# Kernel tuning notes

Measured on AMD Instinct MI355X. Metric: run time of the kernel, lower is better.

Reference implementation:

```python
import jax, jax.numpy as jnp
import numpy as np

B, S, D_MODEL = 2, 2048, 1024
HEADS = 16
DK = D_MODEL // HEADS  # 64
Q_RANK, RANK = 6, 2
ROPE_BASE = 10000.0


def _xavier(key, shape):
    # torch nn.init.xavier_uniform_ on weight (out,in); stored here as (in,out)
    fan_in, fan_out = shape
    a = (6.0 / (fan_in + fan_out)) ** 0.5
    return jax.random.uniform(key, shape, jnp.float32, -a, a)


def setup_inputs() -> dict:
    key = jax.random.key(0)
    ks = jax.random.split(key, 10)
    inp = {
        "q": jax.random.normal(ks[0], (B, S, D_MODEL), jnp.float32),
        "k": jax.random.normal(ks[1], (B, S, D_MODEL), jnp.float32),
        "v": jax.random.normal(ks[2], (B, S, D_MODEL), jnp.float32),
        # causal mask; mask==0 -> -inf in scores
        "mask": jnp.tril(jnp.ones((S, S), dtype=bool))[None, None],
        "W_Aq": _xavier(ks[3], (D_MODEL, Q_RANK * HEADS)),
        "W_Ak": _xavier(ks[4], (D_MODEL, RANK * HEADS)),
        "W_Av": _xavier(ks[5], (D_MODEL, RANK * HEADS)),
        "W_Bq": _xavier(ks[6], (D_MODEL, Q_RANK * DK)),
        "W_Bk": _xavier(ks[7], (D_MODEL, RANK * DK)),
        "W_Bv": _xavier(ks[8], (D_MODEL, RANK * DK)),
        "Wo": _xavier(ks[9], (D_MODEL, D_MODEL)),
    }
    return inp


def _rotary_cos_sin(seq_len, dim):
    inv_freq = 1.0 / (ROPE_BASE ** (jnp.arange(0, dim, 2, dtype=jnp.float32) / dim))
    freqs = jnp.outer(jnp.arange(seq_len, dtype=jnp.float32), inv_freq)  # [S, dim/2]
    return jnp.cos(freqs)[None, :, None, :], jnp.sin(freqs)[None, :, None, :]


def _apply_rotary(x, cos, sin):
    # x: [B, S, R, dk]; rotate-half style RoPE
    d = x.shape[-1] // 2
    x1, x2 = x[..., :d], x[..., d:]
    return jnp.concatenate([x1 * cos + x2 * sin, -x1 * sin + x2 * cos], axis=-1)


def reference(q, k, v, mask, W_Aq, W_Ak, W_Av, W_Bq, W_Bk, W_Bv, Wo):
    Bn, Sn, D = q.shape
    # low-rank factor projections
    A_q = (q @ W_Aq).reshape(Bn, Sn, HEADS, Q_RANK)
    A_k = (k @ W_Ak).reshape(Bn, Sn, HEADS, RANK)
    A_v = (v @ W_Av).reshape(Bn, Sn, HEADS, RANK)
    B_q = (q @ W_Bq).reshape(Bn, Sn, Q_RANK, DK)
    B_k = (k @ W_Bk).reshape(Bn, Sn, RANK, DK)
    B_v = (v @ W_Bv).reshape(Bn, Sn, RANK, DK)
    cos, sin = _rotary_cos_sin(Sn, DK)
    B_q = _apply_rotary(B_q, cos, sin)
    B_k = _apply_rotary(B_k, cos, sin)
    # reconstruct per-head q/k/v: [B,H,S,dk]
    qh = jnp.einsum("bshr,bsrd->bhsd", A_q, B_q) / Q_RANK
    kh = jnp.einsum("bshr,bsrd->bhsd", A_k, B_k) / RANK
    vh = jnp.einsum("bshr,bsrd->bhsd", A_v, B_v) / RANK
    # NOTE: original divides by d_k (not sqrt(d_k)) -- faithful to source
    score = jnp.einsum("bhqd,bhkd->bhqk", qh, kh) / DK
    score = jnp.where(mask, score, -jnp.inf)
    # dropout is identity (eval / dropout=0.0)
    att = jax.nn.softmax(score, axis=-1)
    out = jnp.einsum("bhqk,bhkd->bqhd", att, vh).reshape(Bn, Sn, D)
    return out @ Wo
```

## Files before the change

kernel.cpp:

```cpp
#include <hip/hip_runtime.h>
#include <hip/hip_bf16.h>


typedef __attribute__((ext_vector_type(8))) short short8;
typedef __attribute__((ext_vector_type(4))) float floatx4;

#define MFMA16(a, b, c) __builtin_amdgcn_mfma_f32_16x16x32_bf16(a, b, c, 0, 0, 0)

__device__ __forceinline__ float b2f(short s) {
    unsigned int u = ((unsigned int)(unsigned short)s) << 16;
    float f; __builtin_memcpy(&f, &u, 4); return f;
}
__device__ __forceinline__ unsigned short bfbits(float x) {
    __hip_bfloat16 h = __float2bfloat16(x);
    unsigned short u; __builtin_memcpy(&u, &h, 2); return u;
}

__device__ __forceinline__ float wsrc(int n, int k,
                                      const float* __restrict__ Aq, const float* __restrict__ Bq,
                                      const float* __restrict__ Ak, const float* __restrict__ Bk,
                                      const float* __restrict__ Av, const float* __restrict__ Bv,
                                      const float* __restrict__ Wo) {
    if (n < 96) return Aq[(size_t)k * 96 + n];
    if (n < 480) return Bq[(size_t)k * 384 + (n - 96)];
    if (n < 512) return 0.f;
    if (n < 544) return Ak[(size_t)k * 32 + (n - 512)];
    if (n < 672) return Bk[(size_t)k * 128 + (n - 544)];
    if (n < 768) return 0.f;
    if (n < 800) return Av[(size_t)k * 32 + (n - 768)];
    if (n < 928) return Bv[(size_t)k * 128 + (n - 800)];
    if (n < 1024) return 0.f;
    return Wo[(size_t)k * 1024 + (n - 1024)];
}

__global__ __launch_bounds__(256) void pack_wT_kernel(const float* __restrict__ Aq,
                                                      const float* __restrict__ Bq,
                                                      const float* __restrict__ Ak,
                                                      const float* __restrict__ Bk,
                                                      const float* __restrict__ Av,
                                                      const float* __restrict__ Bv,
                                                      const float* __restrict__ Wo,
                                                      __hip_bfloat16* __restrict__ outBase) {
    __shared__ float tile[64][65];
    int k0 = blockIdx.x * 64, n0 = blockIdx.y * 64;
    int tid = threadIdx.x;
#pragma unroll
    for (int p = 0; p < 16; ++p) {
        int idx = p * 256 + tid;
        int kl = idx >> 6, nl = idx & 63;
        tile[kl][nl] = wsrc(n0 + nl, k0 + kl, Aq, Bq, Ak, Bk, Av, Bv, Wo);
    }
    __syncthreads();
#pragma unroll
    for (int p = 0; p < 16; ++p) {
        int idx = p * 256 + tid;
        int nl = idx >> 6, kl = idx & 63;
        outBase[(size_t)(n0 + nl) * 1024 + k0 + kl] = __float2bfloat16(tile[kl][nl]);
    }
}

__global__ __launch_bounds__(256) void gemm3_kernel(const float* __restrict__ q,
                                                    const float* __restrict__ k,
                                                    const float* __restrict__ v,
                                                    const __hip_bfloat16* __restrict__ WT,
                                                    __hip_bfloat16* __restrict__ Pq,
                                                    __hip_bfloat16* __restrict__ Pk,
                                                    __hip_bfloat16* __restrict__ Pv) {
    __shared__ __align__(16) __hip_bfloat16 As[128][72];
    __shared__ __align__(16) __hip_bfloat16 Bs[128][72];
    int lin = blockIdx.x;
    int t = (lin >> 3) & 7;
    int m0 = ((lin & 7) + ((lin >> 6) << 3)) * 128;
    const float* A; __hip_bfloat16* C; int N, n0, wrow;
    if (t < 4)      { A = q; C = Pq; N = 512; n0 = t * 128;        wrow = t * 128; }
    else if (t < 6) { A = k; C = Pk; N = 256; n0 = (t - 4) * 128;  wrow = 512 + (t - 4) * 128; }
    else            { A = v; C = Pv; N = 256; n0 = (t - 6) * 128;  wrow = 768 + (t - 6) * 128; }
    int tid = threadIdx.x;
    int wave = tid >> 6, lane = tid & 63, quad = lane >> 4, l15 = lane & 15;
    int wm = wave >> 1, wn = wave & 1;
    floatx4 acc[4][4];
#pragma unroll
    for (int mt = 0; mt < 4; ++mt)
#pragma unroll
        for (int nt = 0; nt < 4; ++nt) acc[mt][nt] = (floatx4){0.f, 0.f, 0.f, 0.f};

    for (int k0 = 0; k0 < 1024; k0 += 64) {
#pragma unroll
        for (int pp = 0; pp < 8; ++pp) {
            int idx = pp * 256 + tid;
            int row = idx >> 4, c4 = (idx & 15) * 4;
            float4 av = *(const float4*)(A + (size_t)(m0 + row) * 1024 + k0 + c4);
            ushort4 bv;
            bv.x = bfbits(av.x); bv.y = bfbits(av.y); bv.z = bfbits(av.z); bv.w = bfbits(av.w);
            *(ushort4*)&As[row][c4] = bv;
        }
#pragma unroll
        for (int pp = 0; pp < 4; ++pp) {
            int idx = pp * 256 + tid;
            int row = idx >> 3, c8 = (idx & 7) * 8;
            *(uint4*)&Bs[row][c8] = *(const uint4*)(WT + (size_t)(wrow + row) * 1024 + k0 + c8);
        }
        __syncthreads();
#pragma unroll
        for (int ks = 0; ks < 64; ks += 32) {
            short8 af[4], bf[4];
#pragma unroll
            for (int t2 = 0; t2 < 4; ++t2) {
                af[t2] = *(const short8*)&As[wm * 64 + t2 * 16 + l15][ks + quad * 8];
                bf[t2] = *(const short8*)&Bs[wn * 64 + t2 * 16 + l15][ks + quad * 8];
            }
#pragma unroll
            for (int mt = 0; mt < 4; ++mt)
#pragma unroll
                for (int nt = 0; nt < 4; ++nt)
                    acc[mt][nt] = MFMA16(af[mt], bf[nt], acc[mt][nt]);
        }
        __syncthreads();
    }
#pragma unroll
    for (int mt = 0; mt < 4; ++mt)
#pragma unroll
        for (int nt = 0; nt < 4; ++nt)
#pragma unroll
            for (int r = 0; r < 4; ++r) {
                int row = m0 + wm * 64 + mt * 16 + quad * 4 + r;
                int col = n0 + wn * 64 + nt * 16 + l15;
                C[(size_t)row * N + col] = __float2bfloat16(acc[mt][nt][r]);
            }
}

__global__ __launch_bounds__(256) void gemm_out_kernel(const __hip_bfloat16* __restrict__ A,
                                                       const __hip_bfloat16* __restrict__ BT,
                                                       float* __restrict__ C) {
    __shared__ __align__(16) __hip_bfloat16 As[128][72];
    __shared__ __align__(16) __hip_bfloat16 Bs[128][72];
    int lin = blockIdx.x;
    int n0 = ((lin >> 3) & 7) * 128;
    int m0 = ((lin & 7) + ((lin >> 6) << 3)) * 128;
    int tid = threadIdx.x;
    int wave = tid >> 6, lane = tid & 63, quad = lane >> 4, l15 = lane & 15;
    int wm = wave >> 1, wn = wave & 1;
    floatx4 acc[4][4];
#pragma unroll
    for (int mt = 0; mt < 4; ++mt)
#pragma unroll
        for (int nt = 0; nt < 4; ++nt) acc[mt][nt] = (floatx4){0.f, 0.f, 0.f, 0.f};

    for (int k0 = 0; k0 < 1024; k0 += 64) {
#pragma unroll
        for (int pp = 0; pp < 4; ++pp) {
            int idx = pp * 256 + tid;
            int row = idx >> 3, c8 = (idx & 7) * 8;
            *(uint4*)&As[row][c8] = *(const uint4*)(A + (size_t)(m0 + row) * 1024 + k0 + c8);
            *(uint4*)&Bs[row][c8] = *(const uint4*)(BT + (size_t)(n0 + row) * 1024 + k0 + c8);
        }
        __syncthreads();
#pragma unroll
        for (int ks = 0; ks < 64; ks += 32) {
            short8 af[4], bf[4];
#pragma unroll
            for (int t2 = 0; t2 < 4; ++t2) {
                af[t2] = *(const short8*)&As[wm * 64 + t2 * 16 + l15][ks + quad * 8];
                bf[t2] = *(const short8*)&Bs[wn * 64 + t2 * 16 + l15][ks + quad * 8];
            }
#pragma unroll
            for (int mt = 0; mt < 4; ++mt)
#pragma unroll
                for (int nt = 0; nt < 4; ++nt)
                    acc[mt][nt] = MFMA16(af[mt], bf[nt], acc[mt][nt]);
        }
        __syncthreads();
    }
#pragma unroll
    for (int mt = 0; mt < 4; ++mt)
#pragma unroll
        for (int nt = 0; nt < 4; ++nt)
#pragma unroll
            for (int r = 0; r < 4; ++r) {
                int row = m0 + wm * 64 + mt * 16 + quad * 4 + r;
                int col = n0 + wn * 64 + nt * 16 + l15;
                C[(size_t)row * 1024 + col] = acc[mt][nt][r];
            }
}

__global__ __launch_bounds__(256) void combine_vt_kernel(const __hip_bfloat16* __restrict__ Pq,
                                                         const __hip_bfloat16* __restrict__ Pk,
                                                         const __hip_bfloat16* __restrict__ Pv,
                                                         __hip_bfloat16* __restrict__ qh,
                                                         __hip_bfloat16* __restrict__ kh,
                                                         __hip_bfloat16* __restrict__ vT) {
    __shared__ __align__(16) __hip_bfloat16 LAq[16][96];
    __shared__ __align__(16) __hip_bfloat16 LAk[16][32];
    __shared__ __align__(16) __hip_bfloat16 LAv[16][32];
    __shared__ __align__(16) __hip_bfloat16 LBq[16][6][72];
    __shared__ __align__(16) __hip_bfloat16 LBk[16][2][72];
    __shared__ __align__(16) __hip_bfloat16 LBv[16][2][72];
    int tid = threadIdx.x;
    int token0 = blockIdx.x * 16;
    int b = token0 >> 11, s0 = token0 & 2047, bh0 = b * 16;

    for (int i = tid; i < 16 * 512; i += 256) {
        int s = i >> 9, c = i & 511;
        __hip_bfloat16 val = Pq[(size_t)(token0 + s) * 512 + c];
        if (c < 96) LAq[s][c] = val;
        else if (c < 480) LBq[s][(c - 96) >> 6][(c - 96) & 63] = val;
    }
    for (int i = tid; i < 16 * 256; i += 256) {
        int s = i >> 8, c = i & 255;
        __hip_bfloat16 vk = Pk[(size_t)(token0 + s) * 256 + c];
        __hip_bfloat16 vv = Pv[(size_t)(token0 + s) * 256 + c];
        if (c < 32) { LAk[s][c] = vk; LAv[s][c] = vv; }
        else if (c < 160) {
            LBk[s][(c - 32) >> 6][(c - 32) & 63] = vk;
            LBv[s][(c - 32) >> 6][(c - 32) & 63] = vv;
        }
    }
    __syncthreads();
    for (int i = tid; i < 4096; i += 256) {
        int s = i >> 8, rr = (i >> 5) & 7, d = i & 31;
        float inv = __expf(-(float)d * 0.28782313662425576f);
        float rev = (float)(s0 + s) * inv * 0.15915494309189535f;
        rev -= floorf(rev);
        float sn = __builtin_amdgcn_sinf(rev);
        float cs = __builtin_amdgcn_cosf(rev);
        if (rr < 6) {
            float x1 = b2f(*(short*)&LBq[s][rr][d]), x2 = b2f(*(short*)&LBq[s][rr][d + 32]);
            LBq[s][rr][d] = __float2bfloat16(x1 * cs + x2 * sn);
            LBq[s][rr][d + 32] = __float2bfloat16(-x1 * sn + x2 * cs);
        } else {
            int r2 = rr - 6;
            float x1 = b2f(*(short*)&LBk[s][r2][d]), x2 = b2f(*(short*)&LBk[s][r2][d + 32]);
            LBk[s][r2][d] = __float2bfloat16(x1 * cs + x2 * sn);
            LBk[s][r2][d + 32] = __float2bfloat16(-x1 * sn + x2 * cs);
        }
    }
    __syncthreads();
    const float QSCALE = 1.4426950408889634f / 768.0f;
    {
        int s = tid >> 4, h = tid & 15;
        float aq[6], ak0, ak1;
#pragma unroll
        for (int r = 0; r < 6; ++r) aq[r] = b2f(*(short*)&LAq[s][h * 6 + r]);
        ak0 = b2f(*(short*)&LAk[s][h * 2]);
        ak1 = b2f(*(short*)&LAk[s][h * 2 + 1]);
        size_t obase = ((size_t)(bh0 + h) * 2048 + s0 + s) * 64;
#pragma unroll
        for (int dc = 0; dc < 64; dc += 8) {
            float accq[8] = {0, 0, 0, 0, 0, 0, 0, 0};
#pragma unroll
            for (int r = 0; r < 6; ++r) {
                short8 bq = *(const short8*)&LBq[s][r][dc];
#pragma unroll
                for (int e = 0; e < 8; ++e) accq[e] += aq[r] * b2f(bq[e]);
            }
            short8 bk0 = *(const short8*)&LBk[s][0][dc];
            short8 bk1 = *(const short8*)&LBk[s][1][dc];
            ushort outq[8], outk[8];
#pragma unroll
            for (int e = 0; e < 8; ++e) {
                outq[e] = bfbits(accq[e] * QSCALE);
                outk[e] = bfbits(ak0 * b2f(bk0[e]) + ak1 * b2f(bk1[e]));
            }
            *(uint4*)((__hip_bfloat16*)qh + obase + dc) = *(uint4*)outq;
            *(uint4*)((__hip_bfloat16*)kh + obase + dc) = *(uint4*)outk;
        }
    }
    {
        int s = tid & 15, dg = tid >> 4;
#pragma unroll
        for (int h = 0; h < 16; ++h) {
            float a0 = b2f(*(short*)&LAv[s][h * 2]) * 0.5f;
            float a1 = b2f(*(short*)&LAv[s][h * 2 + 1]) * 0.5f;
#pragma unroll
            for (int dd = 0; dd < 4; ++dd) {
                int d = dg * 4 + dd;
                float val = a0 * b2f(*(short*)&LBv[s][0][d]) + a1 * b2f(*(short*)&LBv[s][1][d]);
                vT[((size_t)(bh0 + h) * 64 + d) * 2048 + s0 + s] = __float2bfloat16(val);
            }
        }
    }
}

__global__ __launch_bounds__(256) void flash_kernel(const __hip_bfloat16* __restrict__ qh,
                                                    const __hip_bfloat16* __restrict__ kh,
                                                    const __hip_bfloat16* __restrict__ vT,
                                                    __hip_bfloat16* __restrict__ att) {
    int lin = blockIdx.x + (blockIdx.y << 5);
    int bh = ((lin & 7) << 2) | ((lin >> 3) & 3);
    int qi = 31 - (lin >> 5);
    int tid = threadIdx.x;
    int wave = tid >> 6, lane = tid & 63, quad = lane >> 4, l15 = lane & 15;
    int q0 = qi * 64;
    __shared__ __align__(16) __hip_bfloat16 Ks[64][72];
    __shared__ __align__(16) __hip_bfloat16 Vts[64][72];

    const __hip_bfloat16* qrow = qh + ((size_t)bh * 2048 + q0 + wave * 16 + l15) * 64 + quad * 8;
    short8 aq0 = *(const short8*)(qrow);
    short8 aq1 = *(const short8*)(qrow + 32);

    floatx4 o[4];
#pragma unroll
    for (int nt = 0; nt < 4; ++nt) o[nt] = (floatx4){0.f, 0.f, 0.f, 0.f};
    float rs = 0.f;
    int qloc = wave * 16 + l15;

    for (int j = 0; j <= qi; ++j) {
        int k0 = j * 64;
#pragma unroll
        for (int pp = 0; pp < 2; ++pp) {
            int idx = pp * 256 + tid;
            int row = idx >> 3, c8 = (idx & 7) * 8;
            *(uint4*)&Ks[row][c8] = *(const uint4*)(kh + ((size_t)bh * 2048 + k0 + row) * 64 + c8);
            *(uint4*)&Vts[row][c8] = *(const uint4*)(vT + ((size_t)bh * 64 + row) * 2048 + k0 + c8);
        }
        __syncthreads();

        floatx4 s[4];
#pragma unroll
        for (int nt = 0; nt < 4; ++nt) s[nt] = (floatx4){0.f, 0.f, 0.f, 0.f};
#pragma unroll
        for (int nt = 0; nt < 4; ++nt) {
            short8 bk0 = *(const short8*)&Ks[nt * 16 + l15][quad * 8];
            short8 bk1 = *(const short8*)&Ks[nt * 16 + l15][32 + quad * 8];
            s[nt] = MFMA16(bk0, aq0, s[nt]);
            s[nt] = MFMA16(bk1, aq1, s[nt]);
        }
        if (j == qi) {
#pragma unroll
            for (int nt = 0; nt < 4; ++nt) {
                int kbase = nt * 16 + quad * 4;
#pragma unroll
                for (int r = 0; r < 4; ++r)
                    if (kbase + r > qloc) s[nt][r] = -__builtin_inff();
            }
        }
        float pv[4][4];
#pragma unroll
        for (int nt = 0; nt < 4; ++nt)
#pragma unroll
            for (int r = 0; r < 4; ++r) {
                pv[nt][r] = exp2f(s[nt][r]);
                rs += pv[nt][r];
            }
        union { ushort u[8]; short8 v; } p0, p1;
#pragma unroll
        for (int r = 0; r < 4; ++r) {
            p0.u[r]     = bfbits(pv[0][r]);
            p0.u[4 + r] = bfbits(pv[1][r]);
            p1.u[r]     = bfbits(pv[2][r]);
            p1.u[4 + r] = bfbits(pv[3][r]);
        }
#pragma unroll
        for (int nt = 0; nt < 4; ++nt) {
            int vr = nt * 16 + l15;
            union { ushort4 h[2]; short8 v; } x0, x1;
            x0.h[0] = *(const ushort4*)&Vts[vr][quad * 4];
            x0.h[1] = *(const ushort4*)&Vts[vr][16 + quad * 4];
            x1.h[0] = *(const ushort4*)&Vts[vr][32 + quad * 4];
            x1.h[1] = *(const ushort4*)&Vts[vr][48 + quad * 4];
            o[nt] = MFMA16(x0.v, p0.v, o[nt]);
            o[nt] = MFMA16(x1.v, p1.v, o[nt]);
        }
        __syncthreads();
    }
    rs += __shfl_xor(rs, 16, 64);
    rs += __shfl_xor(rs, 32, 64);
    float inv = 1.0f / rs;
    int b = bh >> 4, h = bh & 15;
    size_t obase = ((size_t)b * 2048 + q0 + wave * 16 + l15) * 1024 + h * 64 + quad * 4;
#pragma unroll
    for (int nt = 0; nt < 4; ++nt) {
        ushort ow[4];
#pragma unroll
        for (int r = 0; r < 4; ++r) ow[r] = bfbits(o[nt][r] * inv);
        *(ushort4*)((__hip_bfloat16*)att + obase + nt * 16) = *(ushort4*)ow;
    }
}

extern "C" void kernel_launch(void* const* d_in, const int* in_sizes, int n_in,
                              void* d_out, int out_size, void* d_ws, size_t ws_size,
                              hipStream_t stream) {
    const float* q = (const float*)d_in[0];
    const float* k = (const float*)d_in[1];
    const float* v = (const float*)d_in[2];
    const float* W_Aq = (const float*)d_in[4];
    const float* W_Ak = (const float*)d_in[5];
    const float* W_Av = (const float*)d_in[6];
    const float* W_Bq = (const float*)d_in[7];
    const float* W_Bk = (const float*)d_in[8];
    const float* W_Bv = (const float*)d_in[9];
    const float* Wo = (const float*)d_in[10];
    float* out = (float*)d_out;

    char* w = (char*)d_ws;
    __hip_bfloat16* qh  = (__hip_bfloat16*)(w + 0);
    __hip_bfloat16* kh  = (__hip_bfloat16*)(w + 8388608);
    __hip_bfloat16* vT  = (__hip_bfloat16*)(w + 16777216);
    __hip_bfloat16* WT  = (__hip_bfloat16*)(w + 25165824);
    __hip_bfloat16* WoT = WT + (size_t)1024 * 1024;
    __hip_bfloat16* Pq  = (__hip_bfloat16*)(w + 29360128);
    __hip_bfloat16* Pk  = (__hip_bfloat16*)(w + 33554432);
    __hip_bfloat16* Pv  = (__hip_bfloat16*)(w + 35651584);
    __hip_bfloat16* att = (__hip_bfloat16*)(w + 37748736);

    pack_wT_kernel<<<dim3(16, 32), 256, 0, stream>>>(W_Aq, W_Bq, W_Ak, W_Bk, W_Av, W_Bv, Wo, WT);
    gemm3_kernel<<<256, 256, 0, stream>>>(q, k, v, WT, Pq, Pk, Pv);
    combine_vt_kernel<<<256, 256, 0, stream>>>(Pq, Pk, Pv, qh, kh, vT);
    flash_kernel<<<dim3(32, 32), 256, 0, stream>>>(qh, kh, vT, att);
    gemm_out_kernel<<<256, 256, 0, stream>>>(att, WoT, out);
}
```

Before: 258.7 us.

## Register-prefetch next tiles in GEMMs and flash; pair causal query tiles per block

Both GEMM kernels now load the next K-slice into registers while MFMAs run on the current shared-memory tile. This replaces the trailing barrier with a leading one so global latency overlaps compute. The flash kernel prefetches the next K/V tile the same way. It also processes two query tiles per block (qi and 31-qi), so every block does the same causal work and the grid halves to 512 blocks. The trade-offs are higher register pressure, possibly lower occupancy, and fewer blocks in flight for the attention kernel.

```diff
diff --git a/kernel.cpp b/kernel.cpp
--- a/kernel.cpp
+++ b/kernel.cpp
@@ -78,29 +78,37 @@
     int tid = threadIdx.x;
     int wave = tid >> 6, lane = tid & 63, quad = lane >> 4, l15 = lane & 15;
     int wm = wave >> 1, wn = wave & 1;
+    int arow = tid >> 4, ac4 = (tid & 15) * 4;
+    int brow = tid >> 3, bc8 = (tid & 7) * 8;
     floatx4 acc[4][4];
 #pragma unroll
     for (int mt = 0; mt < 4; ++mt)
 #pragma unroll
         for (int nt = 0; nt < 4; ++nt) acc[mt][nt] = (floatx4){0.f, 0.f, 0.f, 0.f};
 
+    float4 aR[8]; uint4 bR[4];
+#define G3_LOAD(K0)                                                                       \
+    {                                                                                     \
+        _Pragma("unroll") for (int pp = 0; pp < 8; ++pp)                                  \
+            aR[pp] = *(const float4*)(A + (size_t)(m0 + pp * 16 + arow) * 1024 + (K0) + ac4); \
+        _Pragma("unroll") for (int pp = 0; pp < 4; ++pp)                                  \
+            bR[pp] = *(const uint4*)(WT + (size_t)(wrow + pp * 32 + brow) * 1024 + (K0) + bc8); \
+    }
+    G3_LOAD(0);
     for (int k0 = 0; k0 < 1024; k0 += 64) {
+        __syncthreads();
 #pragma unroll
         for (int pp = 0; pp < 8; ++pp) {
-            int idx = pp * 256 + tid;
-            int row = idx >> 4, c4 = (idx & 15) * 4;
-            float4 av = *(const float4*)(A + (size_t)(m0 + row) * 1024 + k0 + c4);
             ushort4 bv;
-            bv.x = bfbits(av.x); bv.y = bfbits(av.y); bv.z = bfbits(av.z); bv.w = bfbits(av.w);
-            *(ushort4*)&As[row][c4] = bv;
-        }
-#pragma unroll
-        for (int pp = 0; pp < 4; ++pp) {
-            int idx = pp * 256 + tid;
-            int row = idx >> 3, c8 = (idx & 7) * 8;
-            *(uint4*)&Bs[row][c8] = *(const uint4*)(WT + (size_t)(wrow + row) * 1024 + k0 + c8);
-        }
+            bv.x = bfbits(aR[pp].x); bv.y = bfbits(aR[pp].y);
+            bv.z = bfbits(aR[pp].z); bv.w = bfbits(aR[pp].w);
+            *(ushort4*)&As[pp * 16 + arow][ac4] = bv;
+        }
+#pragma unroll
+        for (int pp = 0; pp < 4; ++pp)
+            *(uint4*)&Bs[pp * 32 + brow][bc8] = bR[pp];
         __syncthreads();
+        if (k0 + 64 < 1024) G3_LOAD(k0 + 64);
 #pragma unroll
         for (int ks = 0; ks < 64; ks += 32) {
             short8 af[4], bf[4];
@@ -115,8 +123,8 @@
                 for (int nt = 0; nt < 4; ++nt)
                     acc[mt][nt] = MFMA16(af[mt], bf[nt], acc[mt][nt]);
         }
-        __syncthreads();
-    }
+    }
+#undef G3_LOAD
 #pragma unroll
     for (int mt = 0; mt < 4; ++mt)
 #pragma unroll
@@ -140,21 +148,31 @@
     int tid = threadIdx.x;
     int wave = tid >> 6, lane = tid & 63, quad = lane >> 4, l15 = lane & 15;
     int wm = wave >> 1, wn = wave & 1;
+    int srow = tid >> 3, sc8 = (tid & 7) * 8;
     floatx4 acc[4][4];
 #pragma unroll
     for (int mt = 0; mt < 4; ++mt)
 #pragma unroll
         for (int nt = 0; nt < 4; ++nt) acc[mt][nt] = (floatx4){0.f, 0.f, 0.f, 0.f};
 
+    uint4 aR[4], bR[4];
+#define GO_LOAD(K0)                                                                        \
+    {                                                                                      \
+        _Pragma("unroll") for (int pp = 0; pp < 4; ++pp) {                                 \
+            aR[pp] = *(const uint4*)(A + (size_t)(m0 + pp * 32 + srow) * 1024 + (K0) + sc8);  \
+            bR[pp] = *(const uint4*)(BT + (size_t)(n0 + pp * 32 + srow) * 1024 + (K0) + sc8); \
+        }                                                                                  \
+    }
+    GO_LOAD(0);
     for (int k0 = 0; k0 < 1024; k0 += 64) {
+        __syncthreads();
 #pragma unroll
         for (int pp = 0; pp < 4; ++pp) {
-            int idx = pp * 256 + tid;
-            int row = idx >> 3, c8 = (idx & 7) * 8;
-            *(uint4*)&As[row][c8] = *(const uint4*)(A + (size_t)(m0 + row) * 1024 + k0 + c8);
-            *(uint4*)&Bs[row][c8] = *(const uint4*)(BT + (size_t)(n0 + row) * 1024 + k0 + c8);
+            *(uint4*)&As[pp * 32 + srow][sc8] = aR[pp];
+            *(uint4*)&Bs[pp * 32 + srow][sc8] = bR[pp];
         }
         __syncthreads();
+        if (k0 + 64 < 1024) GO_LOAD(k0 + 64);
 #pragma unroll
         for (int ks = 0; ks < 64; ks += 32) {
             short8 af[4], bf[4];
@@ -169,8 +187,8 @@
                 for (int nt = 0; nt < 4; ++nt)
                     acc[mt][nt] = MFMA16(af[mt], bf[nt], acc[mt][nt]);
         }
-        __syncthreads();
-    }
+    }
+#undef GO_LOAD
 #pragma unroll
     for (int mt = 0; mt < 4; ++mt)
 #pragma unroll
@@ -287,94 +305,111 @@
                                                     __hip_bfloat16* __restrict__ att) {
     int lin = blockIdx.x + (blockIdx.y << 5);
     int bh = ((lin & 7) << 2) | ((lin >> 3) & 3);
-    int qi = 31 - (lin >> 5);
+    int tpair = lin >> 5;
     int tid = threadIdx.x;
     int wave = tid >> 6, lane = tid & 63, quad = lane >> 4, l15 = lane & 15;
-    int q0 = qi * 64;
     __shared__ __align__(16) __hip_bfloat16 Ks[64][72];
     __shared__ __align__(16) __hip_bfloat16 Vts[64][72];
 
-    const __hip_bfloat16* qrow = qh + ((size_t)bh * 2048 + q0 + wave * 16 + l15) * 64 + quad * 8;
-    short8 aq0 = *(const short8*)(qrow);
-    short8 aq1 = *(const short8*)(qrow + 32);
-
-    floatx4 o[4];
-#pragma unroll
-    for (int nt = 0; nt < 4; ++nt) o[nt] = (floatx4){0.f, 0.f, 0.f, 0.f};
-    float rs = 0.f;
-    int qloc = wave * 16 + l15;
-
-    for (int j = 0; j <= qi; ++j) {
-        int k0 = j * 64;
-#pragma unroll
-        for (int pp = 0; pp < 2; ++pp) {
-            int idx = pp * 256 + tid;
-            int row = idx >> 3, c8 = (idx & 7) * 8;
-            *(uint4*)&Ks[row][c8] = *(const uint4*)(kh + ((size_t)bh * 2048 + k0 + row) * 64 + c8);
-            *(uint4*)&Vts[row][c8] = *(const uint4*)(vT + ((size_t)bh * 64 + row) * 2048 + k0 + c8);
-        }
-        __syncthreads();
-
-        floatx4 s[4];
-#pragma unroll
-        for (int nt = 0; nt < 4; ++nt) s[nt] = (floatx4){0.f, 0.f, 0.f, 0.f};
+    int row0 = tid >> 3, col = (tid & 7) * 8;
+    int row1 = 32 + row0;
+    const size_t khb = (size_t)bh * 2048 * 64;
+    const size_t vtb = (size_t)bh * 64 * 2048;
+    uint4 sk0, sk1, sv0, sv1;
+#define FL_ISSUE(J)                                                            \
+    {                                                                          \
+        int k0_ = (J) * 64;                                                    \
+        sk0 = *(const uint4*)(kh + khb + (size_t)(k0_ + row0) * 64 + col);     \
+        sk1 = *(const uint4*)(kh + khb + (size_t)(k0_ + row1) * 64 + col);     \
+        sv0 = *(const uint4*)(vT + vtb + (size_t)row0 * 2048 + k0_ + col);     \
+        sv1 = *(const uint4*)(vT + vtb + (size_t)row1 * 2048 + k0_ + col);     \
+    }
+
+    for (int pass = 0; pass < 2; ++pass) {
+        int qi = pass ? tpair : (31 - tpair);
+        int q0 = qi * 64;
+        const __hip_bfloat16* qrow =
+            qh + ((size_t)bh * 2048 + q0 + wave * 16 + l15) * 64 + quad * 8;
+        short8 aq0 = *(const short8*)(qrow);
+        short8 aq1 = *(const short8*)(qrow + 32);
+
+        floatx4 o[4];
+#pragma unroll
+        for (int nt = 0; nt < 4; ++nt) o[nt] = (floatx4){0.f, 0.f, 0.f, 0.f};
+        float rs = 0.f;
+        int qloc = wave * 16 + l15;
+
+        FL_ISSUE(0);
+        for (int j = 0; j <= qi; ++j) {
+            __syncthreads();
+            *(uint4*)&Ks[row0][col] = sk0;
+            *(uint4*)&Ks[row1][col] = sk1;
+            *(uint4*)&Vts[row0][col] = sv0;
+            *(uint4*)&Vts[row1][col] = sv1;
+            __syncthreads();
+            if (j < qi) FL_ISSUE(j + 1);
+
+            floatx4 s[4];
+#pragma unroll
+            for (int nt = 0; nt < 4; ++nt) s[nt] = (floatx4){0.f, 0.f, 0.f, 0.f};
+#pragma unroll
+            for (int nt = 0; nt < 4; ++nt) {
+                short8 bk0 = *(const short8*)&Ks[nt * 16 + l15][quad * 8];
+                short8 bk1 = *(const short8*)&Ks[nt * 16 + l15][32 + quad * 8];
+                s[nt] = MFMA16(bk0, aq0, s[nt]);
+                s[nt] = MFMA16(bk1, aq1, s[nt]);
+            }
+            if (j == qi) {
+#pragma unroll
+                for (int nt = 0; nt < 4; ++nt) {
+                    int kbase = nt * 16 + quad * 4;
+#pragma unroll
+                    for (int r = 0; r < 4; ++r)
+                        if (kbase + r > qloc) s[nt][r] = -__builtin_inff();
+                }
+            }
+            float pv[4][4];
+#pragma unroll
+            for (int nt = 0; nt < 4; ++nt)
+#pragma unroll
+                for (int r = 0; r < 4; ++r) {
+                    pv[nt][r] = exp2f(s[nt][r]);
+                    rs += pv[nt][r];
+                }
+            union { ushort u[8]; short8 v; } p0, p1;
+#pragma unroll
+            for (int r = 0; r < 4; ++r) {
+                p0.u[r]     = bfbits(pv[0][r]);
+                p0.u[4 + r] = bfbits(pv[1][r]);
+                p1.u[r]     = bfbits(pv[2][r]);
+                p1.u[4 + r] = bfbits(pv[3][r]);
+            }
+#pragma unroll
+            for (int nt = 0; nt < 4; ++nt) {
+                int vr = nt * 16 + l15;
+                union { ushort4 h[2]; short8 v; } x0, x1;
+                x0.h[0] = *(const ushort4*)&Vts[vr][quad * 4];
+                x0.h[1] = *(const ushort4*)&Vts[vr][16 + quad * 4];
+                x1.h[0] = *(const ushort4*)&Vts[vr][32 + quad * 4];
+                x1.h[1] = *(const ushort4*)&Vts[vr][48 + quad * 4];
+                o[nt] = MFMA16(x0.v, p0.v, o[nt]);
+                o[nt] = MFMA16(x1.v, p1.v, o[nt]);
+            }
+        }
+        rs += __shfl_xor(rs, 16, 64);
+        rs += __shfl_xor(rs, 32, 64);
+        float inv = 1.0f / rs;
+        int b = bh >> 4, h = bh & 15;
+        size_t obase = ((size_t)b * 2048 + q0 + wave * 16 + l15) * 1024 + h * 64 + quad * 4;
 #pragma unroll
         for (int nt = 0; nt < 4; ++nt) {
-            short8 bk0 = *(const short8*)&Ks[nt * 16 + l15][quad * 8];
-            short8 bk1 = *(const short8*)&Ks[nt * 16 + l15][32 + quad * 8];
-            s[nt] = MFMA16(bk0, aq0, s[nt]);
-            s[nt] = MFMA16(bk1, aq1, s[nt]);
-        }
-        if (j == qi) {
-#pragma unroll
-            for (int nt = 0; nt < 4; ++nt) {
-                int kbase = nt * 16 + quad * 4;
-#pragma unroll
-                for (int r = 0; r < 4; ++r)
-                    if (kbase + r > qloc) s[nt][r] = -__builtin_inff();
-            }
-        }
-        float pv[4][4];
-#pragma unroll
-        for (int nt = 0; nt < 4; ++nt)
-#pragma unroll
-            for (int r = 0; r < 4; ++r) {
-                pv[nt][r] = exp2f(s[nt][r]);
-                rs += pv[nt][r];
-            }
-        union { ushort u[8]; short8 v; } p0, p1;
-#pragma unroll
-        for (int r = 0; r < 4; ++r) {
-            p0.u[r]     = bfbits(pv[0][r]);
-            p0.u[4 + r] = bfbits(pv[1][r]);
-            p1.u[r]     = bfbits(pv[2][r]);
-            p1.u[4 + r] = bfbits(pv[3][r]);
-        }
-#pragma unroll
-        for (int nt = 0; nt < 4; ++nt) {
-            int vr = nt * 16 + l15;
-            union { ushort4 h[2]; short8 v; } x0, x1;
-            x0.h[0] = *(const ushort4*)&Vts[vr][quad * 4];
-            x0.h[1] = *(const ushort4*)&Vts[vr][16 + quad * 4];
-            x1.h[0] = *(const ushort4*)&Vts[vr][32 + quad * 4];
-            x1.h[1] = *(const ushort4*)&Vts[vr][48 + quad * 4];
-            o[nt] = MFMA16(x0.v, p0.v, o[nt]);
-            o[nt] = MFMA16(x1.v, p1.v, o[nt]);
-        }
-        __syncthreads();
-    }
-    rs += __shfl_xor(rs, 16, 64);
-    rs += __shfl_xor(rs, 32, 64);
-    float inv = 1.0f / rs;
-    int b = bh >> 4, h = bh & 15;
-    size_t obase = ((size_t)b * 2048 + q0 + wave * 16 + l15) * 1024 + h * 64 + quad * 4;
-#pragma unroll
-    for (int nt = 0; nt < 4; ++nt) {
-        ushort ow[4];
-#pragma unroll
-        for (int r = 0; r < 4; ++r) ow[r] = bfbits(o[nt][r] * inv);
-        *(ushort4*)((__hip_bfloat16*)att + obase + nt * 16) = *(ushort4*)ow;
-    }
+            ushort ow[4];
+#pragma unroll
+            for (int r = 0; r < 4; ++r) ow[r] = bfbits(o[nt][r] * inv);
+            *(ushort4*)((__hip_bfloat16*)att + obase + nt * 16) = *(ushort4*)ow;
+        }
+    }
+#undef FL_ISSUE
 }
 
 extern "C" void kernel_launch(void* const* d_in, const int* in_sizes, int n_in,
@@ -406,6 +441,6 @@
     pack_wT_kernel<<<dim3(16, 32), 256, 0, stream>>>(W_Aq, W_Bq, W_Ak, W_Bk, W_Av, W_Bv, Wo, WT);
     gemm3_kernel<<<256, 256, 0, stream>>>(q, k, v, WT, Pq, Pk, Pv);
     combine_vt_kernel<<<256, 256, 0, stream>>>(Pq, Pk, Pv, qh, kh, vT);
-    flash_kernel<<<dim3(32, 32), 256, 0, stream>>>(qh, kh, vT, att);
+    flash_kernel<<<dim3(32, 16), 256, 0, stream>>>(qh, kh, vT, att);
     gemm_out_kernel<<<256, 256, 0, stream>>>(att, WoT, out);
 }
```

Result: slower. 271.8 us (+5.1%).

## Halve GEMM M-tiles, pair causal q-tiles per flash block, prefetch K/V

Applied to the files above, without the earlier changes.

The projection and output GEMMs move to 64x128 tiles and launch twice as many blocks, so more of the GPU's compute units get work at this problem size. The flash kernel now gives each block two complementary query tiles (qi and 31-qi), which balances causal work across blocks and halves the grid. It also prefetches the next K/V tile into registers before the current tile's compute, so global loads overlap with MFMA work. The costs are less reuse per GEMM tile and more register pressure in the flash loop.

```diff
diff --git a/kernel.cpp b/kernel.cpp
--- a/kernel.cpp
+++ b/kernel.cpp
@@ -66,27 +66,27 @@
                                                     __hip_bfloat16* __restrict__ Pq,
                                                     __hip_bfloat16* __restrict__ Pk,
                                                     __hip_bfloat16* __restrict__ Pv) {
-    __shared__ __align__(16) __hip_bfloat16 As[128][72];
+    __shared__ __align__(16) __hip_bfloat16 As[64][72];
     __shared__ __align__(16) __hip_bfloat16 Bs[128][72];
     int lin = blockIdx.x;
     int t = (lin >> 3) & 7;
-    int m0 = ((lin & 7) + ((lin >> 6) << 3)) * 128;
+    int mi = (lin & 7) + ((lin >> 6) << 3);
+    int m0 = mi * 64;
     const float* A; __hip_bfloat16* C; int N, n0, wrow;
     if (t < 4)      { A = q; C = Pq; N = 512; n0 = t * 128;        wrow = t * 128; }
     else if (t < 6) { A = k; C = Pk; N = 256; n0 = (t - 4) * 128;  wrow = 512 + (t - 4) * 128; }
     else            { A = v; C = Pv; N = 256; n0 = (t - 6) * 128;  wrow = 768 + (t - 6) * 128; }
     int tid = threadIdx.x;
     int wave = tid >> 6, lane = tid & 63, quad = lane >> 4, l15 = lane & 15;
-    int wm = wave >> 1, wn = wave & 1;
-    floatx4 acc[4][4];
+    floatx4 acc[4][2];
 #pragma unroll
     for (int mt = 0; mt < 4; ++mt)
 #pragma unroll
-        for (int nt = 0; nt < 4; ++nt) acc[mt][nt] = (floatx4){0.f, 0.f, 0.f, 0.f};
+        for (int nt = 0; nt < 2; ++nt) acc[mt][nt] = (floatx4){0.f, 0.f, 0.f, 0.f};
 
     for (int k0 = 0; k0 < 1024; k0 += 64) {
 #pragma unroll
-        for (int pp = 0; pp < 8; ++pp) {
+        for (int pp = 0; pp < 4; ++pp) {
             int idx = pp * 256 + tid;
             int row = idx >> 4, c4 = (idx & 15) * 4;
             float4 av = *(const float4*)(A + (size_t)(m0 + row) * 1024 + k0 + c4);
@@ -103,16 +103,17 @@
         __syncthreads();
 #pragma unroll
         for (int ks = 0; ks < 64; ks += 32) {
-            short8 af[4], bf[4];
-#pragma unroll
-            for (int t2 = 0; t2 < 4; ++t2) {
-                af[t2] = *(const short8*)&As[wm * 64 + t2 * 16 + l15][ks + quad * 8];
-                bf[t2] = *(const short8*)&Bs[wn * 64 + t2 * 16 + l15][ks + quad * 8];
-            }
+            short8 af[4], bf[2];
 #pragma unroll
             for (int mt = 0; mt < 4; ++mt)
-#pragma unroll
-                for (int nt = 0; nt < 4; ++nt)
+                af[mt] = *(const short8*)&As[mt * 16 + l15][ks + quad * 8];
+#pragma unroll
+            for (int nt = 0; nt < 2; ++nt)
+                bf[nt] = *(const short8*)&Bs[wave * 32 + nt * 16 + l15][ks + quad * 8];
+#pragma unroll
+            for (int mt = 0; mt < 4; ++mt)
+#pragma unroll
+                for (int nt = 0; nt < 2; ++nt)
                     acc[mt][nt] = MFMA16(af[mt], bf[nt], acc[mt][nt]);
         }
         __syncthreads();
@@ -120,11 +121,11 @@
 #pragma unroll
     for (int mt = 0; mt < 4; ++mt)
 #pragma unroll
-        for (int nt = 0; nt < 4; ++nt)
+        for (int nt = 0; nt < 2; ++nt)
 #pragma unroll
             for (int r = 0; r < 4; ++r) {
-                int row = m0 + wm * 64 + mt * 16 + quad * 4 + r;
-                int col = n0 + wn * 64 + nt * 16 + l15;
+                int row = m0 + mt * 16 + quad * 4 + r;
+                int col = n0 + wave * 32 + nt * 16 + l15;
                 C[(size_t)row * N + col] = __float2bfloat16(acc[mt][nt][r]);
             }
 }
@@ -132,41 +133,47 @@
 __global__ __launch_bounds__(256) void gemm_out_kernel(const __hip_bfloat16* __restrict__ A,
                                                        const __hip_bfloat16* __restrict__ BT,
                                                        float* __restrict__ C) {
-    __shared__ __align__(16) __hip_bfloat16 As[128][72];
+    __shared__ __align__(16) __hip_bfloat16 As[64][72];
     __shared__ __align__(16) __hip_bfloat16 Bs[128][72];
     int lin = blockIdx.x;
     int n0 = ((lin >> 3) & 7) * 128;
-    int m0 = ((lin & 7) + ((lin >> 6) << 3)) * 128;
+    int mi = (lin & 7) + ((lin >> 6) << 3);
+    int m0 = mi * 64;
     int tid = threadIdx.x;
     int wave = tid >> 6, lane = tid & 63, quad = lane >> 4, l15 = lane & 15;
-    int wm = wave >> 1, wn = wave & 1;
-    floatx4 acc[4][4];
+    floatx4 acc[4][2];
 #pragma unroll
     for (int mt = 0; mt < 4; ++mt)
 #pragma unroll
-        for (int nt = 0; nt < 4; ++nt) acc[mt][nt] = (floatx4){0.f, 0.f, 0.f, 0.f};
+        for (int nt = 0; nt < 2; ++nt) acc[mt][nt] = (floatx4){0.f, 0.f, 0.f, 0.f};
 
     for (int k0 = 0; k0 < 1024; k0 += 64) {
+#pragma unroll
+        for (int pp = 0; pp < 2; ++pp) {
+            int idx = pp * 256 + tid;
+            int row = idx >> 3, c8 = (idx & 7) * 8;
+            *(uint4*)&As[row][c8] = *(const uint4*)(A + (size_t)(m0 + row) * 1024 + k0 + c8);
+        }
 #pragma unroll
         for (int pp = 0; pp < 4; ++pp) {
             int idx = pp * 256 + tid;
             int row = idx >> 3, c8 = (idx & 7) * 8;
-            *(uint4*)&As[row][c8] = *(const uint4*)(A + (size_t)(m0 + row) * 1024 + k0 + c8);
             *(uint4*)&Bs[row][c8] = *(const uint4*)(BT + (size_t)(n0 + row) * 1024 + k0 + c8);
         }
         __syncthreads();
 #pragma unroll
         for (int ks = 0; ks < 64; ks += 32) {
-            short8 af[4], bf[4];
-#pragma unroll
-            for (int t2 = 0; t2 < 4; ++t2) {
-                af[t2] = *(const short8*)&As[wm * 64 + t2 * 16 + l15][ks + quad * 8];
-                bf[t2] = *(const short8*)&Bs[wn * 64 + t2 * 16 + l15][ks + quad * 8];
-            }
+            short8 af[4], bf[2];
 #pragma unroll
             for (int mt = 0; mt < 4; ++mt)
-#pragma unroll
-                for (int nt = 0; nt < 4; ++nt)
+                af[mt] = *(const short8*)&As[mt * 16 + l15][ks + quad * 8];
+#pragma unroll
+            for (int nt = 0; nt < 2; ++nt)
+                bf[nt] = *(const short8*)&Bs[wave * 32 + nt * 16 + l15][ks + quad * 8];
+#pragma unroll
+            for (int mt = 0; mt < 4; ++mt)
+#pragma unroll
+                for (int nt = 0; nt < 2; ++nt)
                     acc[mt][nt] = MFMA16(af[mt], bf[nt], acc[mt][nt]);
         }
         __syncthreads();
@@ -174,11 +181,11 @@
 #pragma unroll
     for (int mt = 0; mt < 4; ++mt)
 #pragma unroll
-        for (int nt = 0; nt < 4; ++nt)
+        for (int nt = 0; nt < 2; ++nt)
 #pragma unroll
             for (int r = 0; r < 4; ++r) {
-                int row = m0 + wm * 64 + mt * 16 + quad * 4 + r;
-                int col = n0 + wn * 64 + nt * 16 + l15;
+                int row = m0 + mt * 16 + quad * 4 + r;
+                int col = n0 + wave * 32 + nt * 16 + l15;
                 C[(size_t)row * 1024 + col] = acc[mt][nt][r];
             }
 }
@@ -287,94 +294,111 @@
                                                     __hip_bfloat16* __restrict__ att) {
     int lin = blockIdx.x + (blockIdx.y << 5);
     int bh = ((lin & 7) << 2) | ((lin >> 3) & 3);
-    int qi = 31 - (lin >> 5);
+    int tpair = lin >> 5;
     int tid = threadIdx.x;
     int wave = tid >> 6, lane = tid & 63, quad = lane >> 4, l15 = lane & 15;
-    int q0 = qi * 64;
     __shared__ __align__(16) __hip_bfloat16 Ks[64][72];
     __shared__ __align__(16) __hip_bfloat16 Vts[64][72];
 
-    const __hip_bfloat16* qrow = qh + ((size_t)bh * 2048 + q0 + wave * 16 + l15) * 64 + quad * 8;
-    short8 aq0 = *(const short8*)(qrow);
-    short8 aq1 = *(const short8*)(qrow + 32);
-
-    floatx4 o[4];
-#pragma unroll
-    for (int nt = 0; nt < 4; ++nt) o[nt] = (floatx4){0.f, 0.f, 0.f, 0.f};
-    float rs = 0.f;
-    int qloc = wave * 16 + l15;
-
-    for (int j = 0; j <= qi; ++j) {
-        int k0 = j * 64;
-#pragma unroll
-        for (int pp = 0; pp < 2; ++pp) {
-            int idx = pp * 256 + tid;
-            int row = idx >> 3, c8 = (idx & 7) * 8;
-            *(uint4*)&Ks[row][c8] = *(const uint4*)(kh + ((size_t)bh * 2048 + k0 + row) * 64 + c8);
-            *(uint4*)&Vts[row][c8] = *(const uint4*)(vT + ((size_t)bh * 64 + row) * 2048 + k0 + c8);
-        }
-        __syncthreads();
-
-        floatx4 s[4];
-#pragma unroll
-        for (int nt = 0; nt < 4; ++nt) s[nt] = (floatx4){0.f, 0.f, 0.f, 0.f};
+    int row0 = tid >> 3, col = (tid & 7) * 8;
+    int row1 = 32 + row0;
+    const size_t khb = (size_t)bh * 2048 * 64;
+    const size_t vtb = (size_t)bh * 64 * 2048;
+    uint4 sk0, sk1, sv0, sv1;
+#define FL_ISSUE(J)                                                            \
+    {                                                                          \
+        int k0_ = (J) * 64;                                                    \
+        sk0 = *(const uint4*)(kh + khb + (size_t)(k0_ + row0) * 64 + col);     \
+        sk1 = *(const uint4*)(kh + khb + (size_t)(k0_ + row1) * 64 + col);     \
+        sv0 = *(const uint4*)(vT + vtb + (size_t)row0 * 2048 + k0_ + col);     \
+        sv1 = *(const uint4*)(vT + vtb + (size_t)row1 * 2048 + k0_ + col);     \
+    }
+
+    for (int pass = 0; pass < 2; ++pass) {
+        int qi = pass ? tpair : (31 - tpair);
+        int q0 = qi * 64;
+        const __hip_bfloat16* qrow =
+            qh + ((size_t)bh * 2048 + q0 + wave * 16 + l15) * 64 + quad * 8;
+        short8 aq0 = *(const short8*)(qrow);
+        short8 aq1 = *(const short8*)(qrow + 32);
+
+        floatx4 o[4];
+#pragma unroll
+        for (int nt = 0; nt < 4; ++nt) o[nt] = (floatx4){0.f, 0.f, 0.f, 0.f};
+        float rs = 0.f;
+        int qloc = wave * 16 + l15;
+
+        FL_ISSUE(0);
+        for (int j = 0; j <= qi; ++j) {
+            __syncthreads();
+            *(uint4*)&Ks[row0][col] = sk0;
+            *(uint4*)&Ks[row1][col] = sk1;
+            *(uint4*)&Vts[row0][col] = sv0;
+            *(uint4*)&Vts[row1][col] = sv1;
+            __syncthreads();
+            if (j < qi) FL_ISSUE(j + 1);
+
+            floatx4 s[4];
+#pragma unroll
+            for (int nt = 0; nt < 4; ++nt) s[nt] = (floatx4){0.f, 0.f, 0.f, 0.f};
+#pragma unroll
+            for (int nt = 0; nt < 4; ++nt) {
+                short8 bk0 = *(const short8*)&Ks[nt * 16 + l15][quad * 8];
+                short8 bk1 = *(const short8*)&Ks[nt * 16 + l15][32 + quad * 8];
+                s[nt] = MFMA16(bk0, aq0, s[nt]);
+                s[nt] = MFMA16(bk1, aq1, s[nt]);
+            }
+            if (j == qi) {
+#pragma unroll
+                for (int nt = 0; nt < 4; ++nt) {
+                    int kbase = nt * 16 + quad * 4;
+#pragma unroll
+                    for (int r = 0; r < 4; ++r)
+                        if (kbase + r > qloc) s[nt][r] = -__builtin_inff();
+                }
+            }
+            float pv[4][4];
+#pragma unroll
+            for (int nt = 0; nt < 4; ++nt)
+#pragma unroll
+                for (int r = 0; r < 4; ++r) {
+                    pv[nt][r] = exp2f(s[nt][r]);
+                    rs += pv[nt][r];
+                }
+            union { ushort u[8]; short8 v; } p0, p1;
+#pragma unroll
+            for (int r = 0; r < 4; ++r) {
+                p0.u[r]     = bfbits(pv[0][r]);
+                p0.u[4 + r] = bfbits(pv[1][r]);
+                p1.u[r]     = bfbits(pv[2][r]);
+                p1.u[4 + r] = bfbits(pv[3][r]);
+            }
+#pragma unroll
+            for (int nt = 0; nt < 4; ++nt) {
+                int vr = nt * 16 + l15;
+                union { ushort4 h[2]; short8 v; } x0, x1;
+                x0.h[0] = *(const ushort4*)&Vts[vr][quad * 4];
+                x0.h[1] = *(const ushort4*)&Vts[vr][16 + quad * 4];
+                x1.h[0] = *(const ushort4*)&Vts[vr][32 + quad * 4];
+                x1.h[1] = *(const ushort4*)&Vts[vr][48 + quad * 4];
+                o[nt] = MFMA16(x0.v, p0.v, o[nt]);
+                o[nt] = MFMA16(x1.v, p1.v, o[nt]);
+            }
+        }
+        rs += __shfl_xor(rs, 16, 64);
+        rs += __shfl_xor(rs, 32, 64);
+        float inv = 1.0f / rs;
+        int b = bh >> 4, h = bh & 15;
+        size_t obase = ((size_t)b * 2048 + q0 + wave * 16 + l15) * 1024 + h * 64 + quad * 4;
 #pragma unroll
         for (int nt = 0; nt < 4; ++nt) {
-            short8 bk0 = *(const short8*)&Ks[nt * 16 + l15][quad * 8];
-            short8 bk1 = *(const short8*)&Ks[nt * 16 + l15][32 + quad * 8];
-            s[nt] = MFMA16(bk0, aq0, s[nt]);
-            s[nt] = MFMA16(bk1, aq1, s[nt]);
-        }
-        if (j == qi) {
-#pragma unroll
-            for (int nt = 0; nt < 4; ++nt) {
-                int kbase = nt * 16 + quad * 4;
-#pragma unroll
-                for (int r = 0; r < 4; ++r)
-                    if (kbase + r > qloc) s[nt][r] = -__builtin_inff();
-            }
-        }
-        float pv[4][4];
-#pragma unroll
-        for (int nt = 0; nt < 4; ++nt)
-#pragma unroll
-            for (int r = 0; r < 4; ++r) {
-                pv[nt][r] = exp2f(s[nt][r]);
-                rs += pv[nt][r];
-            }
-        union { ushort u[8]; short8 v; } p0, p1;
-#pragma unroll
-        for (int r = 0; r < 4; ++r) {
-            p0.u[r]     = bfbits(pv[0][r]);
-            p0.u[4 + r] = bfbits(pv[1][r]);
-            p1.u[r]     = bfbits(pv[2][r]);
-            p1.u[4 + r] = bfbits(pv[3][r]);
-        }
-#pragma unroll
-        for (int nt = 0; nt < 4; ++nt) {
-            int vr = nt * 16 + l15;
-            union { ushort4 h[2]; short8 v; } x0, x1;
-            x0.h[0] = *(const ushort4*)&Vts[vr][quad * 4];
-            x0.h[1] = *(const ushort4*)&Vts[vr][16 + quad * 4];
-            x1.h[0] = *(const ushort4*)&Vts[vr][32 + quad * 4];
-            x1.h[1] = *(const ushort4*)&Vts[vr][48 + quad * 4];
-            o[nt] = MFMA16(x0.v, p0.v, o[nt]);
-            o[nt] = MFMA16(x1.v, p1.v, o[nt]);
-        }
-        __syncthreads();
-    }
-    rs += __shfl_xor(rs, 16, 64);
-    rs += __shfl_xor(rs, 32, 64);
-    float inv = 1.0f / rs;
-    int b = bh >> 4, h = bh & 15;
-    size_t obase = ((size_t)b * 2048 + q0 + wave * 16 + l15) * 1024 + h * 64 + quad * 4;
-#pragma unroll
-    for (int nt = 0; nt < 4; ++nt) {
-        ushort ow[4];
-#pragma unroll
-        for (int r = 0; r < 4; ++r) ow[r] = bfbits(o[nt][r] * inv);
-        *(ushort4*)((__hip_bfloat16*)att + obase + nt * 16) = *(ushort4*)ow;
-    }
+            ushort ow[4];
+#pragma unroll
+            for (int r = 0; r < 4; ++r) ow[r] = bfbits(o[nt][r] * inv);
+            *(ushort4*)((__hip_bfloat16*)att + obase + nt * 16) = *(ushort4*)ow;
+        }
+    }
+#undef FL_ISSUE
 }
 
 extern "C" void kernel_launch(void* const* d_in, const int* in_sizes, int n_in,
@@ -404,8 +428,8 @@
     __hip_bfloat16* att = (__hip_bfloat16*)(w + 37748736);
 
     pack_wT_kernel<<<dim3(16, 32), 256, 0, stream>>>(W_Aq, W_Bq, W_Ak, W_Bk, W_Av, W_Bv, Wo, WT);
-    gemm3_kernel<<<256, 256, 0, stream>>>(q, k, v, WT, Pq, Pk, Pv);
+    gemm3_kernel<<<512, 256, 0, stream>>>(q, k, v, WT, Pq, Pk, Pv);
     combine_vt_kernel<<<256, 256, 0, stream>>>(Pq, Pk, Pv, qh, kh, vT);
-    flash_kernel<<<dim3(32, 32), 256, 0, stream>>>(qh, kh, vT, att);
-    gemm_out_kernel<<<256, 256, 0, stream>>>(att, WoT, out);
-}
+    flash_kernel<<<dim3(32, 16), 256, 0, stream>>>(qh, kh, vT, att);
+    gemm_out_kernel<<<512, 256, 0, stream>>>(att, WoT, out);
+}
```

Result: faster. 229.9 us (-11.1%).
